# Kernel tuning notes

Hardware: AMD Instinct MI355X
Metric: run time of the kernel (lower is better)

The kernel has to match this reference:

```python
import jax, jax.numpy as jnp
import numpy as np

N_VAR, N_CON, N_REG = 200_000, 100_000, 50_000
D, OUT = 128, 128
E_ADJ, E_T, E_G = 1_000_000, 500_000, 500_000
EPS = 1e-5


def setup_inputs() -> dict:
    key = jax.random.key(0)
    ks = jax.random.split(key, 16)
    s = 1.0 / np.sqrt(D)
    lin = lambda k: jax.random.uniform(k, (D, OUT), jnp.float32, -s, s)
    return {
        "x_var": jax.random.normal(ks[0], (N_VAR, D), jnp.float32),
        "x_con": jax.random.normal(ks[1], (N_CON, D), jnp.float32),
        "x_region": jax.random.normal(ks[2], (N_REG, D), jnp.float32),
        "src_adj": jax.random.randint(ks[3], (E_ADJ,), 0, N_VAR, jnp.int64 if jax.config.x64_enabled else jnp.int32),
        "dst_adj": jax.random.randint(ks[4], (E_ADJ,), 0, N_VAR, jnp.int32),
        "src_touch": jax.random.randint(ks[5], (E_T,), 0, N_VAR, jnp.int32),
        "dst_touch": jax.random.randint(ks[6], (E_T,), 0, N_CON, jnp.int32),
        "src_groups": jax.random.randint(ks[7], (E_G,), 0, N_REG, jnp.int32),
        "dst_groups": jax.random.randint(ks[8], (E_G,), 0, N_VAR, jnp.int32),
        "W_rel_adj": lin(ks[9]), "b_adj": jnp.zeros((OUT,), jnp.float32), "W_root_adj": lin(ks[10]),
        "W_rel_touch": lin(ks[11]), "b_touch": jnp.zeros((OUT,), jnp.float32), "W_root_touch": lin(ks[12]),
        "W_rel_groups": lin(ks[13]), "b_groups": jnp.zeros((OUT,), jnp.float32), "W_root_groups": lin(ks[14]),
        "gn_w_var": jnp.ones((OUT,), jnp.float32), "gn_b_var": jnp.zeros((OUT,), jnp.float32), "gn_ms_var": jnp.ones((OUT,), jnp.float32),
        "gn_w_con": jnp.ones((OUT,), jnp.float32), "gn_b_con": jnp.zeros((OUT,), jnp.float32), "gn_ms_con": jnp.ones((OUT,), jnp.float32),
    }


def _graph_conv(x_src, x_dst, src, dst, W_rel, b_rel, W_root):
    # PyG GraphConv: lin_rel(sum_{j->i} x_j) + lin_root(x_i); aggregate BEFORE linear.
    agg = jax.ops.segment_sum(x_src[src], dst, num_segments=x_dst.shape[0])
    return agg @ W_rel + b_rel + x_dst @ W_root


def _graph_norm_relu(x, w, b, mean_scale):
    # PyG GraphNorm with batch=None (single graph): per-feature stats over nodes.
    mu = jnp.mean(x, axis=0)
    xc = x - mean_scale * mu
    var = jnp.mean(xc * xc, axis=0)
    return jax.nn.relu(w * xc * jax.lax.rsqrt(var + EPS) + b)


def reference(x_var, x_con, x_region,
              src_adj, dst_adj, src_touch, dst_touch, src_groups, dst_groups,
              W_rel_adj, b_adj, W_root_adj,
              W_rel_touch, b_touch, W_root_touch,
              W_rel_groups, b_groups, W_root_groups,
              gn_w_var, gn_b_var, gn_ms_var,
              gn_w_con, gn_b_con, gn_ms_con):
    # HeteroConv(aggr='sum'): 'var' receives from 'adj' (var->var) and 'groups' (region->var)
    out_var = (_graph_conv(x_var, x_var, src_adj, dst_adj, W_rel_adj, b_adj, W_root_adj)
               + _graph_conv(x_region, x_var, src_groups, dst_groups, W_rel_groups, b_groups, W_root_groups))
    out_con = _graph_conv(x_var, x_con, src_touch, dst_touch, W_rel_touch, b_touch, W_root_touch)
    out_var = _graph_norm_relu(out_var, gn_w_var, gn_b_var, gn_ms_var)
    out_con = _graph_norm_relu(out_con, gn_w_con, gn_b_con, gn_ms_con)
    return out_var, out_con
```

## Files before the change

kernel.cpp:

```cpp
#include <hip/hip_runtime.h>
#include <hip/hip_bf16.h>

#define D 128
#define CAP 40

typedef __attribute__((ext_vector_type(8))) short bf16x8;
typedef __attribute__((ext_vector_type(4))) float f32x4;

__device__ __forceinline__ void atomAddF(float* p, float v) { unsafeAtomicAdd(p, v); }

__device__ __forceinline__ unsigned short f2bf(float f) {
    __hip_bfloat16 h = __float2bfloat16(f);
    return *reinterpret_cast<unsigned short*>(&h);
}
__device__ __forceinline__ float bf2f(unsigned int u16) {
    unsigned int x = u16 << 16;
    return *reinterpret_cast<float*>(&x);
}

__global__ void cast_bf16(const float* __restrict__ in, unsigned short* __restrict__ out, long n4) {
    long i = (long)blockIdx.x * blockDim.x + threadIdx.x;
    if (i >= n4) return;
    float4 v = ((const float4*)in)[i];
    ushort4 o;
    o.x = f2bf(v.x); o.y = f2bf(v.y); o.z = f2bf(v.z); o.w = f2bf(v.w);
    ((ushort4*)out)[i] = o;
}

__global__ void prep_weights(const float* __restrict__ Wra, const float* __restrict__ Wrg,
                             const float* __restrict__ Wrt, const float* __restrict__ Wroot_t,
                             const float* __restrict__ Wroot_a, const float* __restrict__ Wroot_g,
                             const float* __restrict__ ba, const float* __restrict__ bg,
                             unsigned short* __restrict__ Wt_adj, unsigned short* __restrict__ Wt_g,
                             unsigned short* __restrict__ Wt_t, unsigned short* __restrict__ Wt_root_t,
                             unsigned short* __restrict__ Wt_sum, float* __restrict__ bsum) {
    int i = blockIdx.x * blockDim.x + threadIdx.x;
    if (i < D * D) {
        int k = i >> 7, n = i & 127;
        int ti = n * D + k;
        Wt_adj[ti]    = f2bf(Wra[i]);
        Wt_g[ti]      = f2bf(Wrg[i]);
        Wt_t[ti]      = f2bf(Wrt[i]);
        Wt_root_t[ti] = f2bf(Wroot_t[i]);
        Wt_sum[ti]    = f2bf(Wroot_a[i] + Wroot_g[i]);
    }
    if (i < D) bsum[i] = ba[i] + bg[i];
}

__global__ void fill_buckets(const int* __restrict__ src, const int* __restrict__ dst, int E,
                             int* __restrict__ cnt, int* __restrict__ buckets,
                             int* __restrict__ ovf, int* __restrict__ ovf_cnt) {
    int e = blockIdx.x * blockDim.x + threadIdx.x;
    if (e >= E) return;
    int d = dst[e];
    int p = atomicAdd(&cnt[d], 1);
    if (p < CAP) buckets[(long)d * CAP + p] = src[e];
    else         ovf[atomicAdd(ovf_cnt, 1)] = e;
}

__launch_bounds__(256)
__global__ void pull_agg(const unsigned short* __restrict__ y,
                         const int* __restrict__ cnt, const int* __restrict__ buckets,
                         const int* __restrict__ src, const int* __restrict__ dst,
                         const int* __restrict__ ovf, const int* __restrict__ ovf_cnt,
                         unsigned short* __restrict__ agg, int N) {
    int wid = (int)(((long)blockIdx.x * blockDim.x + threadIdx.x) >> 6);
    int lane = threadIdx.x & 63;
    if (wid >= N) return;
    const int half = lane >> 5;
    const int hl = lane & 31;
    const long colOff = (long)hl * 4;

    int m = cnt[wid];
    int mc = m > CAP ? CAP : m;
    int idx = (lane < mc) ? buckets[(long)wid * CAP + lane] : 0;

    float acc0 = 0.f, acc1 = 0.f, acc2 = 0.f, acc3 = 0.f;

    for (int j = 0; j < mc; j += 4) {
        int e0 = j + half;
        int e1 = j + 2 + half;
        int s0 = __shfl(idx, e0, 64);
        int s1 = __shfl(idx, e1, 64);
        uint2 r0 = *(const uint2*)(y + (long)s0 * D + colOff);
        uint2 r1 = *(const uint2*)(y + (long)s1 * D + colOff);
        if (e0 >= mc) { r0.x = 0u; r0.y = 0u; }
        if (e1 >= mc) { r1.x = 0u; r1.y = 0u; }
        acc0 += bf2f(r0.x & 0xffffu) + bf2f(r1.x & 0xffffu);
        acc1 += bf2f(r0.x >> 16)     + bf2f(r1.x >> 16);
        acc2 += bf2f(r0.y & 0xffffu) + bf2f(r1.y & 0xffffu);
        acc3 += bf2f(r0.y >> 16)     + bf2f(r1.y >> 16);
    }

    if (m > CAP) {
        int oc = *ovf_cnt;
        for (int i = 0; i < oc; ++i) {
            int e = ovf[i];
            if (dst[e] == wid && half == 0) {
                int s = src[e];
                uint2 r = *(const uint2*)(y + (long)s * D + colOff);
                acc0 += bf2f(r.x & 0xffffu);
                acc1 += bf2f(r.x >> 16);
                acc2 += bf2f(r.y & 0xffffu);
                acc3 += bf2f(r.y >> 16);
            }
        }
    }

    acc0 += __shfl_xor(acc0, 32, 64);
    acc1 += __shfl_xor(acc1, 32, 64);
    acc2 += __shfl_xor(acc2, 32, 64);
    acc3 += __shfl_xor(acc3, 32, 64);

    if (half == 0) {
        uint2 o;
        o.x = (unsigned int)f2bf(acc0) | ((unsigned int)f2bf(acc1) << 16);
        o.y = (unsigned int)f2bf(acc2) | ((unsigned int)f2bf(acc3) << 16);
        *(uint2*)(agg + (long)wid * D + colOff) = o;
    }
}

__launch_bounds__(256, 4)
__global__ void gemm_fused(int N,
                           const unsigned short* __restrict__ A0, const unsigned short* __restrict__ Wt0,
                           const unsigned short* __restrict__ A1, const unsigned short* __restrict__ Wt1,
                           const unsigned short* __restrict__ A2, const unsigned short* __restrict__ Wt2,
                           int nTerms,
                           const float* __restrict__ bias, float* __restrict__ out,
                           float* __restrict__ gsum, float* __restrict__ gsq) {
    __shared__ unsigned short lds[2][8192];
    __shared__ float sstat[256];
    const int tx = threadIdx.x;
    sstat[tx] = 0.f;

    const int wave = tx >> 6, lane = tx & 63;
    const int quad = lane >> 4, l16 = lane & 15;
    const int row0 = blockIdx.x * 128;

    const int sA0 = tx, sA1 = tx + 256;
    const int rS0 = sA0 >> 2, qS0 = (sA0 & 3) ^ ((sA0 >> 4) & 3);
    const int rS1 = sA1 >> 2, qS1 = (sA1 & 3) ^ ((sA1 >> 4) & 3);
    long gr0 = (long)row0 + rS0; if (gr0 >= N) gr0 = N - 1;
    long gr1 = (long)row0 + rS1; if (gr1 >= N) gr1 = N - 1;

    f32x4 acc[2][8];
#pragma unroll
    for (int rt = 0; rt < 2; ++rt)
#pragma unroll
        for (int ct = 0; ct < 8; ++ct)
#pragma unroll
            for (int i = 0; i < 4; ++i) acc[rt][ct][i] = 0.f;

    auto stage = [&](int s, int bb) {
        const int t = s >> 2;
        const int k0 = (s & 3) * 32;
        const unsigned short* A = (t == 0) ? A0 : ((t == 1) ? A1 : A2);
        const unsigned short* W = (t == 0) ? Wt0 : ((t == 1) ? Wt1 : Wt2);
        __builtin_amdgcn_global_load_lds(
            (const __attribute__((address_space(1))) unsigned int*)(A + gr0 * D + k0 + qS0 * 8),
            (__attribute__((address_space(3))) unsigned int*)(&lds[bb][sA0 * 8]), 16, 0, 0);
        __builtin_amdgcn_global_load_lds(
            (const __attribute__((address_space(1))) unsigned int*)(A + gr1 * D + k0 + qS1 * 8),
            (__attribute__((address_space(3))) unsigned int*)(&lds[bb][sA1 * 8]), 16, 0, 0);
        __builtin_amdgcn_global_load_lds(
            (const __attribute__((address_space(1))) unsigned int*)(W + (long)rS0 * D + k0 + qS0 * 8),
            (__attribute__((address_space(3))) unsigned int*)(&lds[bb][4096 + sA0 * 8]), 16, 0, 0);
        __builtin_amdgcn_global_load_lds(
            (const __attribute__((address_space(1))) unsigned int*)(W + (long)rS1 * D + k0 + qS1 * 8),
            (__attribute__((address_space(3))) unsigned int*)(&lds[bb][4096 + sA1 * 8]), 16, 0, 0);
    };

    const int xq = (l16 >> 2) & 3;
    const int qx = quad ^ xq;

    auto compute = [&](int cb) {
        const int slotA0 = (wave * 32 + l16) * 4 + qx;
        const int slotA1 = (wave * 32 + 16 + l16) * 4 + qx;
        bf16x8 a0 = *(const bf16x8*)&lds[cb][slotA0 * 8];
        bf16x8 a1 = *(const bf16x8*)&lds[cb][slotA1 * 8];
#pragma unroll
        for (int ct = 0; ct < 8; ++ct) {
            const int slotB = (ct * 16 + l16) * 4 + qx;
            bf16x8 b = *(const bf16x8*)&lds[cb][4096 + slotB * 8];
            acc[0][ct] = __builtin_amdgcn_mfma_f32_16x16x32_bf16(a0, b, acc[0][ct], 0, 0, 0);
            acc[1][ct] = __builtin_amdgcn_mfma_f32_16x16x32_bf16(a1, b, acc[1][ct], 0, 0, 0);
        }
    };

    const int nsteps = nTerms * 4;
    stage(0, 0);
    __syncthreads();
    for (int s = 0; s < nsteps; ++s) {
        const int cb = s & 1;
        if (s + 1 < nsteps) stage(s + 1, cb ^ 1);
        compute(cb);
        __syncthreads();
    }

    float bv[8];
#pragma unroll
    for (int ct = 0; ct < 8; ++ct) bv[ct] = bias[ct * 16 + l16];

    float psum[8], psq[8];
#pragma unroll
    for (int ct = 0; ct < 8; ++ct) { psum[ct] = 0.f; psq[ct] = 0.f; }

#pragma unroll
    for (int rt = 0; rt < 2; ++rt)
#pragma unroll
        for (int i = 0; i < 4; ++i) {
            int row = row0 + wave * 32 + rt * 16 + quad * 4 + i;
            if (row < N) {
#pragma unroll
                for (int ct = 0; ct < 8; ++ct) {
                    float v = acc[rt][ct][i] + bv[ct];
                    out[(size_t)row * D + ct * 16 + l16] = v;
                    psum[ct] += v;
                    psq[ct] += v * v;
                }
            }
        }

#pragma unroll
    for (int ct = 0; ct < 8; ++ct) {
        atomicAdd(&sstat[ct * 16 + l16], psum[ct]);
        atomicAdd(&sstat[128 + ct * 16 + l16], psq[ct]);
    }
    __syncthreads();
    if (tx < 128) {
        atomAddF(&gsum[tx], sstat[tx]);
        atomAddF(&gsq[tx], sstat[128 + tx]);
    }
}

__global__ void finalize_stats(const float* __restrict__ stats,
                               const float* __restrict__ wv, const float* __restrict__ bv, const float* __restrict__ msv,
                               const float* __restrict__ wc, const float* __restrict__ bc, const float* __restrict__ msc,
                               int Nvar, int Ncon,
                               float* __restrict__ scale_var, float* __restrict__ shift_var,
                               float* __restrict__ scale_con, float* __restrict__ shift_con) {
    int tx = threadIdx.x;
    if (tx < 128) {
        float n = (float)Nvar;
        float mu = stats[tx] / n;
        float ex2 = stats[128 + tx] / n;
        float ms = msv[tx];
        float var = ex2 - 2.f * ms * mu * mu + ms * ms * mu * mu;
        float istd = rsqrtf(var + 1e-5f);
        float sc = wv[tx] * istd;
        scale_var[tx] = sc;
        shift_var[tx] = bv[tx] - sc * ms * mu;
    } else if (tx < 256) {
        int t = tx - 128;
        float n = (float)Ncon;
        float mu = stats[256 + t] / n;
        float ex2 = stats[384 + t] / n;
        float ms = msc[t];
        float var = ex2 - 2.f * ms * mu * mu + ms * ms * mu * mu;
        float istd = rsqrtf(var + 1e-5f);
        float sc = wc[t] * istd;
        scale_con[t] = sc;
        shift_con[t] = bc[t] - sc * ms * mu;
    }
}

__global__ void norm_relu(float* __restrict__ buf,
                          const float* __restrict__ scale, const float* __restrict__ shift,
                          long nvec) {
    long i = (long)blockIdx.x * blockDim.x + threadIdx.x;
    if (i >= nvec) return;
    int q = ((int)i & 31) * 4;
    float4 v = *(float4*)(buf + i * 4);
    float4 o;
    o.x = fmaxf(0.f, v.x * scale[q + 0] + shift[q + 0]);
    o.y = fmaxf(0.f, v.y * scale[q + 1] + shift[q + 1]);
    o.z = fmaxf(0.f, v.z * scale[q + 2] + shift[q + 2]);
    o.w = fmaxf(0.f, v.w * scale[q + 3] + shift[q + 3]);
    *(float4*)(buf + i * 4) = o;
}

extern "C" void kernel_launch(void* const* d_in, const int* in_sizes, int n_in,
                              void* d_out, int out_size, void* d_ws, size_t ws_size,
                              hipStream_t stream) {
    const float* x_var = (const float*)d_in[0];
    const float* x_con = (const float*)d_in[1];
    const float* x_reg = (const float*)d_in[2];
    const int* src_adj = (const int*)d_in[3];
    const int* dst_adj = (const int*)d_in[4];
    const int* src_t   = (const int*)d_in[5];
    const int* dst_t   = (const int*)d_in[6];
    const int* src_g   = (const int*)d_in[7];
    const int* dst_g   = (const int*)d_in[8];
    const float* W_rel_adj  = (const float*)d_in[9];
    const float* b_adj      = (const float*)d_in[10];
    const float* W_root_adj = (const float*)d_in[11];
    const float* W_rel_t    = (const float*)d_in[12];
    const float* b_t        = (const float*)d_in[13];
    const float* W_root_t   = (const float*)d_in[14];
    const float* W_rel_g    = (const float*)d_in[15];
    const float* b_g        = (const float*)d_in[16];
    const float* W_root_g   = (const float*)d_in[17];
    const float* gnw_v  = (const float*)d_in[18];
    const float* gnb_v  = (const float*)d_in[19];
    const float* gnms_v = (const float*)d_in[20];
    const float* gnw_c  = (const float*)d_in[21];
    const float* gnb_c  = (const float*)d_in[22];
    const float* gnms_c = (const float*)d_in[23];

    const int Nvar = in_sizes[0] / D;
    const int Ncon = in_sizes[1] / D;
    const int Nreg = in_sizes[2] / D;
    const int Eadj = in_sizes[3];
    const int Et   = in_sizes[5];
    const int Eg   = in_sizes[7];
    const int Emax = Eadj > Et ? (Eadj > Eg ? Eadj : Eg) : (Et > Eg ? Et : Eg);

    char* p = (char*)d_ws;
    unsigned short* xv_bf = (unsigned short*)p; p += (size_t)Nvar * D * 2;
    unsigned short* xc_bf = (unsigned short*)p; p += (size_t)Ncon * D * 2;
    unsigned short* xr_bf = (unsigned short*)p; p += (size_t)Nreg * D * 2;
    unsigned short* agg_adj = (unsigned short*)p; p += (size_t)Nvar * D * 2;
    unsigned short* agg_g   = (unsigned short*)p; p += (size_t)Nvar * D * 2;
    unsigned short* agg_t   = (unsigned short*)p; p += (size_t)Ncon * D * 2;
    int* buckets = (int*)p; p += (size_t)Nvar * CAP * 4;
    int* ovf     = (int*)p; p += (size_t)Emax * 4;
    int* cnt     = (int*)p; p += (size_t)Nvar * 4;
    unsigned short* Wt_adj    = (unsigned short*)p; p += D * D * 2;
    unsigned short* Wt_g      = (unsigned short*)p; p += D * D * 2;
    unsigned short* Wt_t      = (unsigned short*)p; p += D * D * 2;
    unsigned short* Wt_root_t = (unsigned short*)p; p += D * D * 2;
    unsigned short* Wt_sum    = (unsigned short*)p; p += D * D * 2;
    float* bsum  = (float*)p; p += D * 4;
    float* stats = (float*)p; p += 512 * 4;
    float* scale_var = (float*)p; p += D * 4;
    float* shift_var = (float*)p; p += D * 4;
    float* scale_con = (float*)p; p += D * 4;
    float* shift_con = (float*)p; p += D * 4;
    int* ovf_cnt = (int*)p; p += 256;

    float* out_var = (float*)d_out;
    float* out_con = out_var + (size_t)Nvar * D;

    hipMemsetAsync(stats, 0, 512 * sizeof(float), stream);
    prep_weights<<<64, 256, 0, stream>>>(W_rel_adj, W_rel_g, W_rel_t, W_root_t,
                                         W_root_adj, W_root_g, b_adj, b_g,
                                         Wt_adj, Wt_g, Wt_t, Wt_root_t, Wt_sum, bsum);

    cast_bf16<<<(int)(((long)Nvar * 32 + 255) / 256), 256, 0, stream>>>(x_var, xv_bf, (long)Nvar * 32);
    cast_bf16<<<(int)(((long)Ncon * 32 + 255) / 256), 256, 0, stream>>>(x_con, xc_bf, (long)Ncon * 32);
    cast_bf16<<<(int)(((long)Nreg * 32 + 255) / 256), 256, 0, stream>>>(x_reg, xr_bf, (long)Nreg * 32);

    struct G { const unsigned short* xs; const int* src; const int* dst; int E; int Ndst; unsigned short* agg; };
    G graphs[3] = {
        { xv_bf, src_adj, dst_adj, Eadj, Nvar, agg_adj },
        { xr_bf, src_g,   dst_g,   Eg,   Nvar, agg_g   },
        { xv_bf, src_t,   dst_t,   Et,   Ncon, agg_t   },
    };

    for (int gi = 0; gi < 3; ++gi) {
        G& g = graphs[gi];
        hipMemsetAsync(cnt, 0, (size_t)g.Ndst * sizeof(int), stream);
        hipMemsetAsync(ovf_cnt, 0, sizeof(int), stream);
        fill_buckets<<<(g.E + 255) / 256, 256, 0, stream>>>(g.src, g.dst, g.E, cnt, buckets, ovf, ovf_cnt);
        long T = (long)g.Ndst * 64;
        pull_agg<<<(int)((T + 255) / 256), 256, 0, stream>>>(g.xs, cnt, buckets,
                                                             g.src, g.dst, ovf, ovf_cnt,
                                                             g.agg, g.Ndst);
    }

    gemm_fused<<<(Nvar + 127) / 128, 256, 0, stream>>>(Nvar,
        agg_adj, Wt_adj, agg_g, Wt_g, xv_bf, Wt_sum, 3,
        bsum, out_var, stats, stats + 128);
    gemm_fused<<<(Ncon + 127) / 128, 256, 0, stream>>>(Ncon,
        agg_t, Wt_t, xc_bf, Wt_root_t, nullptr, nullptr, 2,
        b_t, out_con, stats + 256, stats + 384);

    finalize_stats<<<1, 256, 0, stream>>>(stats,
        gnw_v, gnb_v, gnms_v, gnw_c, gnb_c, gnms_c,
        Nvar, Ncon, scale_var, shift_var, scale_con, shift_con);

    {
        long nvec = (long)Nvar * 32;
        norm_relu<<<(int)((nvec + 255) / 256), 256, 0, stream>>>(out_var, scale_var, shift_var, nvec);
    }
    {
        long nvec = (long)Ncon * 32;
        norm_relu<<<(int)((nvec + 255) / 256), 256, 0, stream>>>(out_con, scale_con, shift_con, nvec);
    }
}
```

Measured before the change: 809.1 us.

## Merge var/con GEMMs into one launch and load MFMA operands directly from global

Combines the two gemm_fused launches into a single grid, with each block picking the var or con problem from its block index. Drops the double-buffered LDS staging via global_load_lds and has each wave read its A rows and W columns straight from global memory into registers. The stat reduction now shuffles across quads before the LDS atomics, cutting LDS atomic traffic by four. The cost is that W tiles are no longer shared through LDS, so every wave re-reads all of W, and register pressure rises (launch bounds drop from 4 to 3 blocks per SM).

```diff
diff --git a/kernel.cpp b/kernel.cpp
--- a/kernel.cpp
+++ b/kernel.cpp
@@ -120,28 +120,35 @@
     }
 }
 
-__launch_bounds__(256, 4)
-__global__ void gemm_fused(int N,
-                           const unsigned short* __restrict__ A0, const unsigned short* __restrict__ Wt0,
-                           const unsigned short* __restrict__ A1, const unsigned short* __restrict__ Wt1,
-                           const unsigned short* __restrict__ A2, const unsigned short* __restrict__ Wt2,
-                           int nTerms,
-                           const float* __restrict__ bias, float* __restrict__ out,
-                           float* __restrict__ gsum, float* __restrict__ gsq) {
-    __shared__ unsigned short lds[2][8192];
+__launch_bounds__(256, 3)
+__global__ void gemm_fused(int nbVar, int Nvar, int Ncon,
+                           const unsigned short* __restrict__ Av0, const unsigned short* __restrict__ Wv0,
+                           const unsigned short* __restrict__ Av1, const unsigned short* __restrict__ Wv1,
+                           const unsigned short* __restrict__ Av2, const unsigned short* __restrict__ Wv2,
+                           const unsigned short* __restrict__ Ac0, const unsigned short* __restrict__ Wc0,
+                           const unsigned short* __restrict__ Ac1, const unsigned short* __restrict__ Wc1,
+                           const float* __restrict__ biasV, const float* __restrict__ biasC,
+                           float* __restrict__ outV, float* __restrict__ outC,
+                           float* __restrict__ stats) {
     __shared__ float sstat[256];
     const int tx = threadIdx.x;
     sstat[tx] = 0.f;
+    __syncthreads();
+
+    const bool isVar = (int)blockIdx.x < nbVar;
+    const int bid = isVar ? blockIdx.x : blockIdx.x - nbVar;
+    const int N = isVar ? Nvar : Ncon;
+    const float* bias = isVar ? biasV : biasC;
+    float* out = isVar ? outV : outC;
+    float* gsum = stats + (isVar ? 0 : 256);
+    float* gsq = gsum + 128;
 
     const int wave = tx >> 6, lane = tx & 63;
     const int quad = lane >> 4, l16 = lane & 15;
-    const int row0 = blockIdx.x * 128;
-
-    const int sA0 = tx, sA1 = tx + 256;
-    const int rS0 = sA0 >> 2, qS0 = (sA0 & 3) ^ ((sA0 >> 4) & 3);
-    const int rS1 = sA1 >> 2, qS1 = (sA1 & 3) ^ ((sA1 >> 4) & 3);
-    long gr0 = (long)row0 + rS0; if (gr0 >= N) gr0 = N - 1;
-    long gr1 = (long)row0 + rS1; if (gr1 >= N) gr1 = N - 1;
+    const int row0 = bid * 128 + wave * 32;
+
+    long r0 = row0 + l16;      if (r0 >= N) r0 = N - 1;
+    long r1 = row0 + 16 + l16; if (r1 >= N) r1 = N - 1;
 
     f32x4 acc[2][8];
 #pragma unroll
@@ -151,51 +158,28 @@
 #pragma unroll
             for (int i = 0; i < 4; ++i) acc[rt][ct][i] = 0.f;
 
-    auto stage = [&](int s, int bb) {
-        const int t = s >> 2;
-        const int k0 = (s & 3) * 32;
-        const unsigned short* A = (t == 0) ? A0 : ((t == 1) ? A1 : A2);
-        const unsigned short* W = (t == 0) ? Wt0 : ((t == 1) ? Wt1 : Wt2);
-        __builtin_amdgcn_global_load_lds(
-            (const __attribute__((address_space(1))) unsigned int*)(A + gr0 * D + k0 + qS0 * 8),
-            (__attribute__((address_space(3))) unsigned int*)(&lds[bb][sA0 * 8]), 16, 0, 0);
-        __builtin_amdgcn_global_load_lds(
-            (const __attribute__((address_space(1))) unsigned int*)(A + gr1 * D + k0 + qS1 * 8),
-            (__attribute__((address_space(3))) unsigned int*)(&lds[bb][sA1 * 8]), 16, 0, 0);
-        __builtin_amdgcn_global_load_lds(
-            (const __attribute__((address_space(1))) unsigned int*)(W + (long)rS0 * D + k0 + qS0 * 8),
-            (__attribute__((address_space(3))) unsigned int*)(&lds[bb][4096 + sA0 * 8]), 16, 0, 0);
-        __builtin_amdgcn_global_load_lds(
-            (const __attribute__((address_space(1))) unsigned int*)(W + (long)rS1 * D + k0 + qS1 * 8),
-            (__attribute__((address_space(3))) unsigned int*)(&lds[bb][4096 + sA1 * 8]), 16, 0, 0);
-    };
-
-    const int xq = (l16 >> 2) & 3;
-    const int qx = quad ^ xq;
-
-    auto compute = [&](int cb) {
-        const int slotA0 = (wave * 32 + l16) * 4 + qx;
-        const int slotA1 = (wave * 32 + 16 + l16) * 4 + qx;
-        bf16x8 a0 = *(const bf16x8*)&lds[cb][slotA0 * 8];
-        bf16x8 a1 = *(const bf16x8*)&lds[cb][slotA1 * 8];
-#pragma unroll
-        for (int ct = 0; ct < 8; ++ct) {
-            const int slotB = (ct * 16 + l16) * 4 + qx;
-            bf16x8 b = *(const bf16x8*)&lds[cb][4096 + slotB * 8];
-            acc[0][ct] = __builtin_amdgcn_mfma_f32_16x16x32_bf16(a0, b, acc[0][ct], 0, 0, 0);
-            acc[1][ct] = __builtin_amdgcn_mfma_f32_16x16x32_bf16(a1, b, acc[1][ct], 0, 0, 0);
+    auto term = [&](const unsigned short* __restrict__ A, const unsigned short* __restrict__ W) {
+        const unsigned short* a0p = A + r0 * D + quad * 8;
+        const unsigned short* a1p = A + r1 * D + quad * 8;
+        const unsigned short* wp  = W + (long)l16 * D + quad * 8;
+#pragma unroll
+        for (int ks = 0; ks < 4; ++ks) {
+            bf16x8 a0 = *(const bf16x8*)(a0p + ks * 32);
+            bf16x8 a1 = *(const bf16x8*)(a1p + ks * 32);
+            bf16x8 b[8];
+#pragma unroll
+            for (int ct = 0; ct < 8; ++ct)
+                b[ct] = *(const bf16x8*)(wp + ct * 16 * D + ks * 32);
+#pragma unroll
+            for (int ct = 0; ct < 8; ++ct) {
+                acc[0][ct] = __builtin_amdgcn_mfma_f32_16x16x32_bf16(a0, b[ct], acc[0][ct], 0, 0, 0);
+                acc[1][ct] = __builtin_amdgcn_mfma_f32_16x16x32_bf16(a1, b[ct], acc[1][ct], 0, 0, 0);
+            }
         }
     };
 
-    const int nsteps = nTerms * 4;
-    stage(0, 0);
-    __syncthreads();
-    for (int s = 0; s < nsteps; ++s) {
-        const int cb = s & 1;
-        if (s + 1 < nsteps) stage(s + 1, cb ^ 1);
-        compute(cb);
-        __syncthreads();
-    }
+    if (isVar) { term(Av0, Wv0); term(Av1, Wv1); term(Av2, Wv2); }
+    else       { term(Ac0, Wc0); term(Ac1, Wc1); }
 
     float bv[8];
 #pragma unroll
@@ -209,7 +193,7 @@
     for (int rt = 0; rt < 2; ++rt)
 #pragma unroll
         for (int i = 0; i < 4; ++i) {
-            int row = row0 + wave * 32 + rt * 16 + quad * 4 + i;
+            int row = row0 + rt * 16 + quad * 4 + i;
             if (row < N) {
 #pragma unroll
                 for (int ct = 0; ct < 8; ++ct) {
@@ -223,8 +207,17 @@
 
 #pragma unroll
     for (int ct = 0; ct < 8; ++ct) {
-        atomicAdd(&sstat[ct * 16 + l16], psum[ct]);
-        atomicAdd(&sstat[128 + ct * 16 + l16], psq[ct]);
+        psum[ct] += __shfl_xor(psum[ct], 16, 64);
+        psum[ct] += __shfl_xor(psum[ct], 32, 64);
+        psq[ct]  += __shfl_xor(psq[ct], 16, 64);
+        psq[ct]  += __shfl_xor(psq[ct], 32, 64);
+    }
+    if (quad == 0) {
+#pragma unroll
+        for (int ct = 0; ct < 8; ++ct) {
+            atomicAdd(&sstat[ct * 16 + l16], psum[ct]);
+            atomicAdd(&sstat[128 + ct * 16 + l16], psq[ct]);
+        }
     }
     __syncthreads();
     if (tx < 128) {
@@ -368,12 +361,12 @@
                                                              g.agg, g.Ndst);
     }
 
-    gemm_fused<<<(Nvar + 127) / 128, 256, 0, stream>>>(Nvar,
-        agg_adj, Wt_adj, agg_g, Wt_g, xv_bf, Wt_sum, 3,
-        bsum, out_var, stats, stats + 128);
-    gemm_fused<<<(Ncon + 127) / 128, 256, 0, stream>>>(Ncon,
-        agg_t, Wt_t, xc_bf, Wt_root_t, nullptr, nullptr, 2,
-        b_t, out_con, stats + 256, stats + 384);
+    const int nbVar = (Nvar + 127) / 128;
+    const int nbCon = (Ncon + 127) / 128;
+    gemm_fused<<<nbVar + nbCon, 256, 0, stream>>>(nbVar, Nvar, Ncon,
+        agg_adj, Wt_adj, agg_g, Wt_g, xv_bf, Wt_sum,
+        agg_t, Wt_t, xc_bf, Wt_root_t,
+        bsum, b_t, out_var, out_con, stats);
 
     finalize_stats<<<1, 256, 0, stream>>>(stats,
         gnw_v, gnb_v, gnms_v, gnw_c, gnb_c, gnms_c,
```

Result: slower. 852.7 us (+5.4%).

## Merge var/con GEMM launches, use explicit waitcnt barriers, shuffle-reduce stats

Applied to the files above, without the earlier changes.

Folds the two GEMM launches (var and con) into a single grid, with each block picking its problem by block index. This removes one launch and the tail gap between them. The pipeline loop replaces __syncthreads with explicit s_waitcnt vmcnt plus s_barrier, so the prefetch of the next stage can stay in flight while the current one is computed. Column stats are first reduced across quads with wave shuffles, which cuts the LDS atomics by four. The hand-written waitcnt counts rely on the exact number of outstanding loads per stage, and getting that wrong risks races.

```diff
diff --git a/kernel.cpp b/kernel.cpp
--- a/kernel.cpp
+++ b/kernel.cpp
@@ -121,27 +121,37 @@
 }
 
 __launch_bounds__(256, 4)
-__global__ void gemm_fused(int N,
-                           const unsigned short* __restrict__ A0, const unsigned short* __restrict__ Wt0,
-                           const unsigned short* __restrict__ A1, const unsigned short* __restrict__ Wt1,
-                           const unsigned short* __restrict__ A2, const unsigned short* __restrict__ Wt2,
-                           int nTerms,
-                           const float* __restrict__ bias, float* __restrict__ out,
-                           float* __restrict__ gsum, float* __restrict__ gsq) {
+__global__ void gemm_fused(int nbVar, int Nvar, int Ncon,
+                           const unsigned short* __restrict__ Av0, const unsigned short* __restrict__ Wv0,
+                           const unsigned short* __restrict__ Av1, const unsigned short* __restrict__ Wv1,
+                           const unsigned short* __restrict__ Av2, const unsigned short* __restrict__ Wv2,
+                           const unsigned short* __restrict__ Ac0, const unsigned short* __restrict__ Wc0,
+                           const unsigned short* __restrict__ Ac1, const unsigned short* __restrict__ Wc1,
+                           const float* __restrict__ biasV, const float* __restrict__ biasC,
+                           float* __restrict__ outV, float* __restrict__ outC,
+                           float* __restrict__ stats) {
     __shared__ unsigned short lds[2][8192];
     __shared__ float sstat[256];
     const int tx = threadIdx.x;
     sstat[tx] = 0.f;
 
+    const bool isVar = (int)blockIdx.x < nbVar;
+    const int bid = isVar ? (int)blockIdx.x : (int)blockIdx.x - nbVar;
+    const int N = isVar ? Nvar : Ncon;
+    const float* bias = isVar ? biasV : biasC;
+    float* out = isVar ? outV : outC;
+    float* gsum = stats + (isVar ? 0 : 256);
+    float* gsq = gsum + 128;
+
     const int wave = tx >> 6, lane = tx & 63;
     const int quad = lane >> 4, l16 = lane & 15;
-    const int row0 = blockIdx.x * 128;
+    const int brow = bid * 128;
 
     const int sA0 = tx, sA1 = tx + 256;
     const int rS0 = sA0 >> 2, qS0 = (sA0 & 3) ^ ((sA0 >> 4) & 3);
     const int rS1 = sA1 >> 2, qS1 = (sA1 & 3) ^ ((sA1 >> 4) & 3);
-    long gr0 = (long)row0 + rS0; if (gr0 >= N) gr0 = N - 1;
-    long gr1 = (long)row0 + rS1; if (gr1 >= N) gr1 = N - 1;
+    long gr0 = (long)brow + rS0; if (gr0 >= N) gr0 = N - 1;
+    long gr1 = (long)brow + rS1; if (gr1 >= N) gr1 = N - 1;
 
     f32x4 acc[2][8];
 #pragma unroll
@@ -154,8 +164,10 @@
     auto stage = [&](int s, int bb) {
         const int t = s >> 2;
         const int k0 = (s & 3) * 32;
-        const unsigned short* A = (t == 0) ? A0 : ((t == 1) ? A1 : A2);
-        const unsigned short* W = (t == 0) ? Wt0 : ((t == 1) ? Wt1 : Wt2);
+        const unsigned short* A = (t == 0) ? (isVar ? Av0 : Ac0)
+                                : (t == 1) ? (isVar ? Av1 : Ac1) : Av2;
+        const unsigned short* W = (t == 0) ? (isVar ? Wv0 : Wc0)
+                                : (t == 1) ? (isVar ? Wv1 : Wc1) : Wv2;
         __builtin_amdgcn_global_load_lds(
             (const __attribute__((address_space(1))) unsigned int*)(A + gr0 * D + k0 + qS0 * 8),
             (__attribute__((address_space(3))) unsigned int*)(&lds[bb][sA0 * 8]), 16, 0, 0);
@@ -187,14 +199,19 @@
         }
     };
 
-    const int nsteps = nTerms * 4;
+    const int nsteps = (isVar ? 3 : 2) * 4;
     stage(0, 0);
-    __syncthreads();
     for (int s = 0; s < nsteps; ++s) {
         const int cb = s & 1;
-        if (s + 1 < nsteps) stage(s + 1, cb ^ 1);
+        if (s + 1 < nsteps) {
+            stage(s + 1, cb ^ 1);
+            asm volatile("s_waitcnt vmcnt(4)" ::: "memory");
+        } else {
+            asm volatile("s_waitcnt vmcnt(0)" ::: "memory");
+        }
+        asm volatile("s_barrier" ::: "memory");
         compute(cb);
-        __syncthreads();
+        asm volatile("s_barrier" ::: "memory");
     }
 
     float bv[8];
@@ -209,7 +226,7 @@
     for (int rt = 0; rt < 2; ++rt)
 #pragma unroll
         for (int i = 0; i < 4; ++i) {
-            int row = row0 + wave * 32 + rt * 16 + quad * 4 + i;
+            int row = brow + wave * 32 + rt * 16 + quad * 4 + i;
             if (row < N) {
 #pragma unroll
                 for (int ct = 0; ct < 8; ++ct) {
@@ -223,8 +240,17 @@
 
 #pragma unroll
     for (int ct = 0; ct < 8; ++ct) {
-        atomicAdd(&sstat[ct * 16 + l16], psum[ct]);
-        atomicAdd(&sstat[128 + ct * 16 + l16], psq[ct]);
+        psum[ct] += __shfl_xor(psum[ct], 16, 64);
+        psum[ct] += __shfl_xor(psum[ct], 32, 64);
+        psq[ct]  += __shfl_xor(psq[ct], 16, 64);
+        psq[ct]  += __shfl_xor(psq[ct], 32, 64);
+    }
+    if (quad == 0) {
+#pragma unroll
+        for (int ct = 0; ct < 8; ++ct) {
+            atomicAdd(&sstat[ct * 16 + l16], psum[ct]);
+            atomicAdd(&sstat[128 + ct * 16 + l16], psq[ct]);
+        }
     }
     __syncthreads();
     if (tx < 128) {
@@ -368,12 +394,12 @@
                                                              g.agg, g.Ndst);
     }
 
-    gemm_fused<<<(Nvar + 127) / 128, 256, 0, stream>>>(Nvar,
-        agg_adj, Wt_adj, agg_g, Wt_g, xv_bf, Wt_sum, 3,
-        bsum, out_var, stats, stats + 128);
-    gemm_fused<<<(Ncon + 127) / 128, 256, 0, stream>>>(Ncon,
-        agg_t, Wt_t, xc_bf, Wt_root_t, nullptr, nullptr, 2,
-        b_t, out_con, stats + 256, stats + 384);
+    const int nbVar = (Nvar + 127) / 128;
+    const int nbCon = (Ncon + 127) / 128;
+    gemm_fused<<<nbVar + nbCon, 256, 0, stream>>>(nbVar, Nvar, Ncon,
+        agg_adj, Wt_adj, agg_g, Wt_g, xv_bf, Wt_sum,
+        agg_t, Wt_t, xc_bf, Wt_root_t,
+        bsum, b_t, out_var, out_con, stats);
 
     finalize_stats<<<1, 256, 0, stream>>>(stats,
         gnw_v, gnb_v, gnms_v, gnw_c, gnb_c, gnms_c,
```

After: 872.8 us. +7.9%, slower.

## Batch the three graphs' bucketing and aggregation into single launches

Applied to the files above, without the earlier changes.

Merges the three cast kernels, the three fill_buckets/pull_agg pairs, and the two norm_relu launches into single combined launches, giving each graph its own bucket, count and overflow buffers. All zeroing is folded into one memset. It also lowers the bucket capacity from 40 to 32. The aim is to cut launch and memset overhead and fill the GPU better than the small serial per-graph kernels did. The cost is more workspace and more entries spilling to the slow overflow scan, which loops over every overflow entry for each affected node.

```diff
diff --git a/kernel.cpp b/kernel.cpp
--- a/kernel.cpp
+++ b/kernel.cpp
@@ -2,7 +2,7 @@
 #include <hip/hip_bf16.h>
 
 #define D 128
-#define CAP 40
+#define CAP 32
 
 typedef __attribute__((ext_vector_type(8))) short bf16x8;
 typedef __attribute__((ext_vector_type(4))) float f32x4;
@@ -18,13 +18,22 @@
     return *reinterpret_cast<float*>(&x);
 }
 
-__global__ void cast_bf16(const float* __restrict__ in, unsigned short* __restrict__ out, long n4) {
+__global__ void cast_bf16_3(const float* __restrict__ a, long n4a,
+                            const float* __restrict__ b, long n4b,
+                            const float* __restrict__ c, long n4c,
+                            unsigned short* __restrict__ oa,
+                            unsigned short* __restrict__ ob,
+                            unsigned short* __restrict__ oc) {
     long i = (long)blockIdx.x * blockDim.x + threadIdx.x;
-    if (i >= n4) return;
-    float4 v = ((const float4*)in)[i];
+    const float* in; unsigned short* out; long li;
+    if (i < n4a)                { in = a; out = oa; li = i; }
+    else if (i < n4a + n4b)     { in = b; out = ob; li = i - n4a; }
+    else if (i < n4a + n4b + n4c) { in = c; out = oc; li = i - n4a - n4b; }
+    else return;
+    float4 v = ((const float4*)in)[li];
     ushort4 o;
     o.x = f2bf(v.x); o.y = f2bf(v.y); o.z = f2bf(v.z); o.w = f2bf(v.w);
-    ((ushort4*)out)[i] = o;
+    ((ushort4*)out)[li] = o;
 }
 
 __global__ void prep_weights(const float* __restrict__ Wra, const float* __restrict__ Wrg,
@@ -47,43 +56,67 @@
     if (i < D) bsum[i] = ba[i] + bg[i];
 }
 
-__global__ void fill_buckets(const int* __restrict__ src, const int* __restrict__ dst, int E,
-                             int* __restrict__ cnt, int* __restrict__ buckets,
-                             int* __restrict__ ovf, int* __restrict__ ovf_cnt) {
-    int e = blockIdx.x * blockDim.x + threadIdx.x;
-    if (e >= E) return;
-    int d = dst[e];
+__global__ void fill_buckets3(const int* __restrict__ s0, const int* __restrict__ d0, int E0,
+                              const int* __restrict__ s1, const int* __restrict__ d1, int E1,
+                              const int* __restrict__ s2, const int* __restrict__ d2, int E2,
+                              int* __restrict__ cnt0, int* __restrict__ cnt1, int* __restrict__ cnt2,
+                              int* __restrict__ b0, int* __restrict__ b1, int* __restrict__ b2,
+                              int* __restrict__ o0, int* __restrict__ o1, int* __restrict__ o2,
+                              int* __restrict__ ovf_cnt) {
+    long e = (long)blockIdx.x * blockDim.x + threadIdx.x;
+    const int* src; const int* dst; int* cnt; int* bkt; int* ovf; int* oc; int le;
+    if (e < E0)                { src = s0; dst = d0; cnt = cnt0; bkt = b0; ovf = o0; oc = ovf_cnt +  0; le = (int)e; }
+    else if (e < (long)E0 + E1){ src = s1; dst = d1; cnt = cnt1; bkt = b1; ovf = o1; oc = ovf_cnt + 16; le = (int)(e - E0); }
+    else if (e < (long)E0 + E1 + E2) { src = s2; dst = d2; cnt = cnt2; bkt = b2; ovf = o2; oc = ovf_cnt + 32; le = (int)(e - E0 - E1); }
+    else return;
+    int d = dst[le];
     int p = atomicAdd(&cnt[d], 1);
-    if (p < CAP) buckets[(long)d * CAP + p] = src[e];
-    else         ovf[atomicAdd(ovf_cnt, 1)] = e;
+    if (p < CAP) bkt[(long)d * CAP + p] = src[le];
+    else         ovf[atomicAdd(oc, 1)] = le;
 }
 
 __launch_bounds__(256)
-__global__ void pull_agg(const unsigned short* __restrict__ y,
-                         const int* __restrict__ cnt, const int* __restrict__ buckets,
-                         const int* __restrict__ src, const int* __restrict__ dst,
-                         const int* __restrict__ ovf, const int* __restrict__ ovf_cnt,
-                         unsigned short* __restrict__ agg, int N) {
-    int wid = (int)(((long)blockIdx.x * blockDim.x + threadIdx.x) >> 6);
+__global__ void pull_agg3(int Nvar, int Ncon,
+                          const unsigned short* __restrict__ xv, const unsigned short* __restrict__ xr,
+                          const int* __restrict__ cnt0, const int* __restrict__ cnt1, const int* __restrict__ cnt2,
+                          const int* __restrict__ b0, const int* __restrict__ b1, const int* __restrict__ b2,
+                          const int* __restrict__ s0, const int* __restrict__ d0, const int* __restrict__ o0,
+                          const int* __restrict__ s1, const int* __restrict__ d1, const int* __restrict__ o1,
+                          const int* __restrict__ s2, const int* __restrict__ d2, const int* __restrict__ o2,
+                          const int* __restrict__ ovf_cnt,
+                          unsigned short* __restrict__ agg_adj, unsigned short* __restrict__ agg_g,
+                          unsigned short* __restrict__ agg_t) {
+    int gwid = (int)(((long)blockIdx.x * blockDim.x + threadIdx.x) >> 6);
     int lane = threadIdx.x & 63;
-    if (wid >= N) return;
+
+    const unsigned short* y; const int* cnt; const int* bkt;
+    const int* src; const int* dst; const int* ovf; int oc; int wid;
+    unsigned short* agg;
+    if (gwid < Nvar) {
+        y = xv; cnt = cnt0; bkt = b0; src = s0; dst = d0; ovf = o0; oc = ovf_cnt[0];  agg = agg_adj; wid = gwid;
+    } else if (gwid < 2 * Nvar) {
+        y = xr; cnt = cnt1; bkt = b1; src = s1; dst = d1; ovf = o1; oc = ovf_cnt[16]; agg = agg_g;   wid = gwid - Nvar;
+    } else if (gwid < 2 * Nvar + Ncon) {
+        y = xv; cnt = cnt2; bkt = b2; src = s2; dst = d2; ovf = o2; oc = ovf_cnt[32]; agg = agg_t;   wid = gwid - 2 * Nvar;
+    } else return;
+
     const int half = lane >> 5;
     const int hl = lane & 31;
     const long colOff = (long)hl * 4;
 
     int m = cnt[wid];
     int mc = m > CAP ? CAP : m;
-    int idx = (lane < mc) ? buckets[(long)wid * CAP + lane] : 0;
+    int idx = (lane < mc) ? bkt[(long)wid * CAP + lane] : 0;
 
     float acc0 = 0.f, acc1 = 0.f, acc2 = 0.f, acc3 = 0.f;
 
     for (int j = 0; j < mc; j += 4) {
         int e0 = j + half;
         int e1 = j + 2 + half;
-        int s0 = __shfl(idx, e0, 64);
-        int s1 = __shfl(idx, e1, 64);
-        uint2 r0 = *(const uint2*)(y + (long)s0 * D + colOff);
-        uint2 r1 = *(const uint2*)(y + (long)s1 * D + colOff);
+        int v0 = __shfl(idx, e0, 64);
+        int v1 = __shfl(idx, e1, 64);
+        uint2 r0 = *(const uint2*)(y + (long)v0 * D + colOff);
+        uint2 r1 = *(const uint2*)(y + (long)v1 * D + colOff);
         if (e0 >= mc) { r0.x = 0u; r0.y = 0u; }
         if (e1 >= mc) { r1.x = 0u; r1.y = 0u; }
         acc0 += bf2f(r0.x & 0xffffu) + bf2f(r1.x & 0xffffu);
@@ -93,7 +126,6 @@
     }
 
     if (m > CAP) {
-        int oc = *ovf_cnt;
         for (int i = 0; i < oc; ++i) {
             int e = ovf[i];
             if (dst[e] == wid && half == 0) {
@@ -264,11 +296,14 @@
     }
 }
 
-__global__ void norm_relu(float* __restrict__ buf,
-                          const float* __restrict__ scale, const float* __restrict__ shift,
-                          long nvec) {
+__global__ void norm_relu2(float* __restrict__ buf,
+                           long nvecVar, long nvecTot,
+                           const float* __restrict__ sv, const float* __restrict__ hv,
+                           const float* __restrict__ sc2, const float* __restrict__ hc) {
     long i = (long)blockIdx.x * blockDim.x + threadIdx.x;
-    if (i >= nvec) return;
+    if (i >= nvecTot) return;
+    const float* scale; const float* shift;
+    if (i < nvecVar) { scale = sv; shift = hv; } else { scale = sc2; shift = hc; }
     int q = ((int)i & 31) * 4;
     float4 v = *(float4*)(buf + i * 4);
     float4 o;
@@ -313,7 +348,6 @@
     const int Eadj = in_sizes[3];
     const int Et   = in_sizes[5];
     const int Eg   = in_sizes[7];
-    const int Emax = Eadj > Et ? (Eadj > Eg ? Eadj : Eg) : (Et > Eg ? Et : Eg);
 
     char* p = (char*)d_ws;
     unsigned short* xv_bf = (unsigned short*)p; p += (size_t)Nvar * D * 2;
@@ -322,50 +356,64 @@
     unsigned short* agg_adj = (unsigned short*)p; p += (size_t)Nvar * D * 2;
     unsigned short* agg_g   = (unsigned short*)p; p += (size_t)Nvar * D * 2;
     unsigned short* agg_t   = (unsigned short*)p; p += (size_t)Ncon * D * 2;
-    int* buckets = (int*)p; p += (size_t)Nvar * CAP * 4;
-    int* ovf     = (int*)p; p += (size_t)Emax * 4;
-    int* cnt     = (int*)p; p += (size_t)Nvar * 4;
+    int* bkt0 = (int*)p; p += (size_t)Nvar * CAP * 4;
+    int* bkt1 = (int*)p; p += (size_t)Nvar * CAP * 4;
+    int* bkt2 = (int*)p; p += (size_t)Ncon * CAP * 4;
+    int* ovf0 = (int*)p; p += (size_t)Eadj * 4;
+    int* ovf1 = (int*)p; p += (size_t)Eg * 4;
+    int* ovf2 = (int*)p; p += (size_t)Et * 4;
     unsigned short* Wt_adj    = (unsigned short*)p; p += D * D * 2;
     unsigned short* Wt_g      = (unsigned short*)p; p += D * D * 2;
     unsigned short* Wt_t      = (unsigned short*)p; p += D * D * 2;
     unsigned short* Wt_root_t = (unsigned short*)p; p += D * D * 2;
     unsigned short* Wt_sum    = (unsigned short*)p; p += D * D * 2;
     float* bsum  = (float*)p; p += D * 4;
-    float* stats = (float*)p; p += 512 * 4;
     float* scale_var = (float*)p; p += D * 4;
     float* shift_var = (float*)p; p += D * 4;
     float* scale_con = (float*)p; p += D * 4;
     float* shift_con = (float*)p; p += D * 4;
-    int* ovf_cnt = (int*)p; p += 256;
+    char* zbase = p;
+    float* stats   = (float*)p; p += 512 * 4;
+    int* ovf_cnt   = (int*)p;   p += 64 * 4;
+    int* cnt0      = (int*)p;   p += (size_t)Nvar * 4;
+    int* cnt1      = (int*)p;   p += (size_t)Nvar * 4;
+    int* cnt2      = (int*)p;   p += (size_t)Ncon * 4;
+    size_t zbytes = (size_t)(p - zbase);
 
     float* out_var = (float*)d_out;
     float* out_con = out_var + (size_t)Nvar * D;
 
-    hipMemsetAsync(stats, 0, 512 * sizeof(float), stream);
+    hipMemsetAsync(zbase, 0, zbytes, stream);
+
     prep_weights<<<64, 256, 0, stream>>>(W_rel_adj, W_rel_g, W_rel_t, W_root_t,
                                          W_root_adj, W_root_g, b_adj, b_g,
                                          Wt_adj, Wt_g, Wt_t, Wt_root_t, Wt_sum, bsum);
 
-    cast_bf16<<<(int)(((long)Nvar * 32 + 255) / 256), 256, 0, stream>>>(x_var, xv_bf, (long)Nvar * 32);
-    cast_bf16<<<(int)(((long)Ncon * 32 + 255) / 256), 256, 0, stream>>>(x_con, xc_bf, (long)Ncon * 32);
-    cast_bf16<<<(int)(((long)Nreg * 32 + 255) / 256), 256, 0, stream>>>(x_reg, xr_bf, (long)Nreg * 32);
-
-    struct G { const unsigned short* xs; const int* src; const int* dst; int E; int Ndst; unsigned short* agg; };
-    G graphs[3] = {
-        { xv_bf, src_adj, dst_adj, Eadj, Nvar, agg_adj },
-        { xr_bf, src_g,   dst_g,   Eg,   Nvar, agg_g   },
-        { xv_bf, src_t,   dst_t,   Et,   Ncon, agg_t   },
-    };
-
-    for (int gi = 0; gi < 3; ++gi) {
-        G& g = graphs[gi];
-        hipMemsetAsync(cnt, 0, (size_t)g.Ndst * sizeof(int), stream);
-        hipMemsetAsync(ovf_cnt, 0, sizeof(int), stream);
-        fill_buckets<<<(g.E + 255) / 256, 256, 0, stream>>>(g.src, g.dst, g.E, cnt, buckets, ovf, ovf_cnt);
-        long T = (long)g.Ndst * 64;
-        pull_agg<<<(int)((T + 255) / 256), 256, 0, stream>>>(g.xs, cnt, buckets,
-                                                             g.src, g.dst, ovf, ovf_cnt,
-                                                             g.agg, g.Ndst);
+    {
+        long n4v = (long)Nvar * 32, n4c = (long)Ncon * 32, n4r = (long)Nreg * 32;
+        long tot = n4v + n4c + n4r;
+        cast_bf16_3<<<(int)((tot + 255) / 256), 256, 0, stream>>>(
+            x_var, n4v, x_con, n4c, x_reg, n4r, xv_bf, xc_bf, xr_bf);
+    }
+
+    {
+        long Etot = (long)Eadj + Eg + Et;
+        fill_buckets3<<<(int)((Etot + 255) / 256), 256, 0, stream>>>(
+            src_adj, dst_adj, Eadj,
+            src_g,   dst_g,   Eg,
+            src_t,   dst_t,   Et,
+            cnt0, cnt1, cnt2, bkt0, bkt1, bkt2, ovf0, ovf1, ovf2, ovf_cnt);
+    }
+
+    {
+        long T = ((long)2 * Nvar + Ncon) * 64;
+        pull_agg3<<<(int)((T + 255) / 256), 256, 0, stream>>>(
+            Nvar, Ncon, xv_bf, xr_bf,
+            cnt0, cnt1, cnt2, bkt0, bkt1, bkt2,
+            src_adj, dst_adj, ovf0,
+            src_g,   dst_g,   ovf1,
+            src_t,   dst_t,   ovf2,
+            ovf_cnt, agg_adj, agg_g, agg_t);
     }
 
     gemm_fused<<<(Nvar + 127) / 128, 256, 0, stream>>>(Nvar,
@@ -380,11 +428,9 @@
         Nvar, Ncon, scale_var, shift_var, scale_con, shift_con);
 
     {
-        long nvec = (long)Nvar * 32;
-        norm_relu<<<(int)((nvec + 255) / 256), 256, 0, stream>>>(out_var, scale_var, shift_var, nvec);
-    }
-    {
-        long nvec = (long)Ncon * 32;
-        norm_relu<<<(int)((nvec + 255) / 256), 256, 0, stream>>>(out_con, scale_con, shift_con, nvec);
-    }
-}
+        long nvecVar = (long)Nvar * 32;
+        long nvecTot = (long)(Nvar + Ncon) * 32;
+        norm_relu2<<<(int)((nvecTot + 255) / 256), 256, 0, stream>>>(
+            out_var, nvecVar, nvecTot, scale_var, shift_var, scale_con, shift_con);
+    }
+}
```

Measured after the change: 837.4 us. 3.5% more time.
